# Kernel optimization log

Hardware: AMD Instinct MI355X
Metric: run time of the kernel (lower is better)

The kernel has to match this reference:

```python
import jax, jax.numpy as jnp
import numpy as np

N_NODES = 50000
N_EDGES = 800000
IN_DIM = 64
HID_DIM = 64
OUT_DIM = 16
N_RELS = 16
N_BASES = 4


def setup_inputs() -> dict:
    key = jax.random.key(0)
    ks = jax.random.split(key, 11)
    feats = jax.random.normal(ks[0], (N_NODES, IN_DIM), dtype=jnp.float32)
    src = jax.random.randint(ks[1], (N_EDGES,), 0, N_NODES, dtype=jnp.int32)
    dst = jax.random.randint(ks[2], (N_EDGES,), 0, N_NODES, dtype=jnp.int32)
    edge_type = jax.random.randint(ks[3], (N_EDGES,), 0, N_RELS, dtype=jnp.int32)
    edge_norm = jax.random.uniform(ks[4], (N_EDGES,), dtype=jnp.float32)
    # basis-decomposed relation weights: W[r] = sum_b coef[r,b] * bases[b]
    bases1 = jax.random.normal(ks[5], (N_BASES, IN_DIM, HID_DIM), dtype=jnp.float32) * (1.0 / np.sqrt(IN_DIM))
    coef1 = jax.random.normal(ks[6], (N_RELS, N_BASES), dtype=jnp.float32)
    bias1 = jnp.zeros((HID_DIM,), dtype=jnp.float32)
    bases2 = jax.random.normal(ks[7], (N_BASES, HID_DIM, OUT_DIM), dtype=jnp.float32) * (1.0 / np.sqrt(HID_DIM))
    coef2 = jax.random.normal(ks[8], (N_RELS, N_BASES), dtype=jnp.float32)
    bias2 = jnp.zeros((OUT_DIM,), dtype=jnp.float32)
    return {"feats": feats, "src": src, "dst": dst, "edge_type": edge_type,
            "edge_norm": edge_norm, "bases1": bases1, "coef1": coef1, "bias1": bias1,
            "bases2": bases2, "coef2": coef2, "bias2": bias2}


def _rel_graph_conv(x, src, dst, edge_type, edge_norm, bases, coef, bias):
    """One RelGraphConv layer (basis decomposition, low-mem: gather coef, not W)."""
    xs = x[src]                                   # [E, in]  gather source feats
    t = jnp.einsum('ei,bio->ebo', xs, bases)      # [E, B, out] per-basis transform
    c = coef[edge_type]                            # [E, B]   per-edge relation coefs
    msg = jnp.einsum('eb,ebo->eo', c, t)          # [E, out]
    msg = msg * edge_norm[:, None]                # apply edge norm
    h = jax.ops.segment_sum(msg, dst, num_segments=N_NODES)  # scatter-add by dst
    return jax.nn.relu(h + bias)                  # bias + activation (dropout=0, eval)


def reference(feats, src, dst, edge_type, edge_norm, bases1, coef1, bias1, bases2, coef2, bias2):
    h = _rel_graph_conv(feats, src, dst, edge_type, edge_norm, bases1, coef1, bias1)
    h = _rel_graph_conv(h, src, dst, edge_type, edge_norm, bases2, coef2, bias2)
    return h
```

## Files before the change

kernel.cpp:

```cpp
#include <hip/hip_runtime.h>

#define N_NODES 50000
#define N_EDGES 800000

typedef __attribute__((ext_vector_type(8))) short bf16x8;
typedef __attribute__((ext_vector_type(4))) float f32x4;

__device__ __forceinline__ unsigned bf16rne(float x) {
  unsigned u = __float_as_uint(x);
  return (u + 0x7FFFu + ((u >> 16) & 1u)) >> 16;
}
__device__ __forceinline__ unsigned packbf2(float a, float b) {
  return bf16rne(a) | (bf16rne(b) << 16);
}
__device__ __forceinline__ float bflo(unsigned u) { return __uint_as_float(u << 16); }
__device__ __forceinline__ float bfhi(unsigned u) { return __uint_as_float(u & 0xFFFF0000u); }

__global__ __launch_bounds__(256) void k_pack(
    const float4* __restrict__ feats4, uint2* __restrict__ xbf,
    const float* __restrict__ bases1, const float* __restrict__ bases2,
    unsigned short* __restrict__ b1T, unsigned short* __restrict__ b2p) {
  if (blockIdx.x < 3125) {
    const int i = blockIdx.x * 256 + threadIdx.x;
    float4 v = feats4[i];
    xbf[i] = make_uint2(packbf2(v.x, v.y), packbf2(v.z, v.w));
  } else {
    for (int idx = threadIdx.x; idx < 64 * 256; idx += 256) {
      int o = idx >> 8, q = idx & 255;
      b1T[idx] = (unsigned short)bf16rne(bases1[q * 64 + o]);
    }
    for (int idx = threadIdx.x; idx < 64 * 64; idx += 256) {
      int j = idx >> 6, k = idx & 63;
      int o = j >> 2, b = j & 3;
      b2p[idx] = (unsigned short)bf16rne(bases2[b * 1024 + k * 16 + o]);
    }
  }
}

#define G_HIST 64
#define CHUNK (N_EDGES / G_HIST)
#define NSLICE 4
#define HBINS (N_NODES / NSLICE)

__global__ __launch_bounds__(512) void k_hist(
    const int* __restrict__ dst, int* __restrict__ rank,
    unsigned short* __restrict__ bh) {
  __shared__ int hist[HBINS];
  const int c = blockIdx.x & (G_HIST - 1);
  const int p = blockIdx.x >> 6;
  const int e0 = c * CHUNK;
  const int lo = p * HBINS;
  for (int i = threadIdx.x; i < HBINS; i += 512) hist[i] = 0;
  __syncthreads();
  for (int i = threadIdx.x; i < CHUNK; i += 512) {
    const int d = dst[e0 + i] - lo;
    if ((unsigned)d < (unsigned)HBINS)
      rank[e0 + i] = atomicAdd(&hist[d], 1);
  }
  __syncthreads();
  for (int i = threadIdx.x; i < HBINS; i += 512)
    bh[(size_t)c * N_NODES + lo + i] = (unsigned short)hist[i];
}

#define NB 512
__global__ __launch_bounds__(512) void k_scan1(
    unsigned short* __restrict__ bh,
    int* __restrict__ rowp, int* __restrict__ bsum) {
  __shared__ unsigned short tile[G_HIST][NB];
  __shared__ int wsum[8];
  const int tid = threadIdx.x;
  const int n0 = blockIdx.x * NB;
  for (int idx = tid; idx < G_HIST * (NB / 4); idx += 512) {
    const int c = idx >> 7, j = idx & 127;
    const int nloc = 4 * j;
    uint2 u = make_uint2(0u, 0u);
    if (n0 + nloc < N_NODES)
      u = *(const uint2*)(bh + (size_t)c * N_NODES + n0 + nloc);
    *(uint2*)&tile[c][nloc] = u;
  }
  __syncthreads();
  int s = 0;
  for (int c = 0; c < G_HIST; ++c) {
    const int cnt = tile[c][tid];
    tile[c][tid] = (unsigned short)s;
    s += cnt;
  }
  __syncthreads();
  for (int idx = tid; idx < G_HIST * (NB / 4); idx += 512) {
    const int c = idx >> 7, j = idx & 127;
    const int nloc = 4 * j;
    if (n0 + nloc < N_NODES)
      *(uint2*)(bh + (size_t)c * N_NODES + n0 + nloc) = *(uint2*)&tile[c][nloc];
  }
  const int lane = tid & 63, wid = tid >> 6;
  int v = (n0 + tid < N_NODES) ? s : 0;
  int incl = v;
#pragma unroll
  for (int off = 1; off < 64; off <<= 1) {
    int t = __shfl_up(incl, off, 64);
    if (lane >= off) incl += t;
  }
  if (lane == 63) wsum[wid] = incl;
  __syncthreads();
  if (tid < 8) {
    int wi = wsum[tid];
#pragma unroll
    for (int off = 1; off < 8; off <<= 1) {
      int t = __shfl_up(wi, off, 64);
      if (lane >= off) wi += t;
    }
    wsum[tid] = wi;
  }
  __syncthreads();
  int woff = (wid > 0) ? wsum[wid - 1] : 0;
  int incl_all = incl + woff;
  if (n0 + tid < N_NODES) rowp[n0 + tid + 1] = incl_all;
  if (tid == NB - 1) bsum[blockIdx.x] = incl_all;
}

__global__ __launch_bounds__(512) void k_scan3(int* __restrict__ rowp,
                                               const int* __restrict__ bsum) {
  __shared__ int s_off;
  const int tid = threadIdx.x;
  if (tid < 64) {
    int v = 0;
    for (int b = tid; b < (int)blockIdx.x; b += 64) v += bsum[b];
#pragma unroll
    for (int off = 32; off >= 1; off >>= 1) v += __shfl_down(v, off, 64);
    if (tid == 0) s_off = v;
  }
  __syncthreads();
  const int i = blockIdx.x * NB + tid;
  if (i < N_NODES) rowp[i + 1] += s_off;
  if (i == 0) rowp[0] = 0;
}

__global__ __launch_bounds__(256) void k_scatter(
    const int* __restrict__ src, const int* __restrict__ dst,
    const int* __restrict__ ety, const float* __restrict__ enorm,
    const int* __restrict__ rowp, const int* __restrict__ rank,
    const unsigned short* __restrict__ bh, unsigned* __restrict__ s_edge) {
  int e = blockIdx.x * 256 + threadIdx.x;
  if (e >= N_EDGES) return;
  const int d = dst[e];
  const int b = e / CHUNK;
  const int pos = rowp[d] + (int)bh[(size_t)b * N_NODES + d] + rank[e];
  unsigned nq = (unsigned)(enorm[e] * 4096.f + 0.5f);
  nq = nq > 4095u ? 4095u : nq;
  s_edge[pos] = (unsigned)src[e] | ((unsigned)ety[e] << 16) | (nq << 20);
}

#define NMSCALE (1.f / 4096.f)

#define ROWB 264
__device__ __forceinline__ void gather_node(
    const int* __restrict__ rowp, const unsigned* __restrict__ s_edge,
    const uint2* __restrict__ xv, const float4* __restrict__ coefLDS,
    unsigned short* __restrict__ uA,
    int node, int m, int lane) {
  const int eslot = lane >> 4, ch4 = lane & 15;
  const int beg = rowp[node], end = rowp[node + 1];
  float4 a0 = {0, 0, 0, 0}, a1 = {0, 0, 0, 0}, a2 = {0, 0, 0, 0}, a3 = {0, 0, 0, 0};
  int j = beg + eslot;
  unsigned rec0 = 0, rec1 = 0;
  uint2 xp = {0, 0};
  if (j < end) rec0 = s_edge[j];
  if (j + 4 < end) rec1 = s_edge[j + 4];
  if (j < end) xp = xv[(rec0 & 0xFFFF) * 16 + ch4];
  while (j < end) {
    unsigned rec2 = 0;
    uint2 xp1 = {0, 0};
    if (j + 8 < end) rec2 = s_edge[j + 8];
    if (j + 4 < end) xp1 = xv[(rec1 & 0xFFFF) * 16 + ch4];
    const float nm = (float)(rec0 >> 20) * NMSCALE;
    const float4 c = coefLDS[(rec0 >> 16) & 15];
    const float w0 = nm * c.x, w1 = nm * c.y, w2 = nm * c.z, w3 = nm * c.w;
    const float x0 = bflo(xp.x), x1 = bfhi(xp.x), x2 = bflo(xp.y), x3 = bfhi(xp.y);
    a0.x += w0 * x0; a0.y += w0 * x1; a0.z += w0 * x2; a0.w += w0 * x3;
    a1.x += w1 * x0; a1.y += w1 * x1; a1.z += w1 * x2; a1.w += w1 * x3;
    a2.x += w2 * x0; a2.y += w2 * x1; a2.z += w2 * x2; a2.w += w2 * x3;
    a3.x += w3 * x0; a3.y += w3 * x1; a3.z += w3 * x2; a3.w += w3 * x3;
    j += 4; rec0 = rec1; rec1 = rec2; xp = xp1;
  }
#define RED1(x) x += __shfl_down(x, 32, 64)
  RED1(a0.x); RED1(a0.y); RED1(a0.z); RED1(a0.w);
  RED1(a1.x); RED1(a1.y); RED1(a1.z); RED1(a1.w);
  RED1(a2.x); RED1(a2.y); RED1(a2.z); RED1(a2.w);
  RED1(a3.x); RED1(a3.y); RED1(a3.z); RED1(a3.w);
#undef RED1
  if (eslot < 2) {
    unsigned short* row = uA + (eslot * 16 + m) * ROWB + 4 * ch4;
    *(uint2*)(row + 0 * 64) = make_uint2(packbf2(a0.x, a0.y), packbf2(a0.z, a0.w));
    *(uint2*)(row + 1 * 64) = make_uint2(packbf2(a1.x, a1.y), packbf2(a1.z, a1.w));
    *(uint2*)(row + 2 * 64) = make_uint2(packbf2(a2.x, a2.y), packbf2(a2.z, a2.w));
    *(uint2*)(row + 3 * 64) = make_uint2(packbf2(a3.x, a3.y), packbf2(a3.z, a3.w));
  }
}

__global__ __launch_bounds__(256) void k_l1_fused(
    const int* __restrict__ rowp, const unsigned* __restrict__ s_edge,
    const uint2* __restrict__ xbf, const float* __restrict__ coef1,
    const unsigned short* __restrict__ b1T,
    const float* __restrict__ bias1,
    const unsigned short* __restrict__ b2p,
    uint2* __restrict__ y2bf) {
  __shared__ __align__(16) unsigned short uA[2 * 16 * ROWB];
  __shared__ float coefs[64];
  __shared__ float cmat[16 * 68];
  const int wid = threadIdx.x >> 6, lane = threadIdx.x & 63;
  if (threadIdx.x < 64) coefs[threadIdx.x] = coef1[threadIdx.x];
  __syncthreads();
  const int nbase = blockIdx.x * 16;
#pragma unroll
  for (int jn = 0; jn < 4; ++jn) {
    const int m = wid * 4 + jn;
    gather_node(rowp, s_edge, xbf, (const float4*)coefs, uA, nbase + m, m, lane);
  }
  __syncthreads();
  const int nloc = lane & 15, kgrp = lane >> 4;
  f32x4 acc1 = {0.f, 0.f, 0.f, 0.f};
#pragma unroll
  for (int ks = 0; ks < 8; ++ks) {
    const int k0 = ks * 32 + kgrp * 8;
    const bf16x8 b = *(const bf16x8*)&b1T[(wid * 16 + nloc) * 256 + k0];
    const bf16x8 aS0 = *(const bf16x8*)&uA[(0 * 16 + nloc) * ROWB + k0];
    acc1 = __builtin_amdgcn_mfma_f32_16x16x32_bf16(aS0, b, acc1, 0, 0, 0);
    const bf16x8 aS1 = *(const bf16x8*)&uA[(1 * 16 + nloc) * ROWB + k0];
    acc1 = __builtin_amdgcn_mfma_f32_16x16x32_bf16(aS1, b, acc1, 0, 0, 0);
  }
  {
    const int o = wid * 16 + nloc;
    const float bs = bias1[o];
#pragma unroll
    for (int r = 0; r < 4; ++r) {
      const int m = (lane >> 4) * 4 + r;
      cmat[m * 68 + o] = fmaxf(acc1[r] + bs, 0.f);
    }
  }
  __syncthreads();
  f32x4 acc2 = {0.f, 0.f, 0.f, 0.f};
#pragma unroll
  for (int ks = 0; ks < 2; ++ks) {
    const int k0 = ks * 32 + kgrp * 8;
    const float4 c0 = *(const float4*)&cmat[nloc * 68 + k0];
    const float4 c1 = *(const float4*)&cmat[nloc * 68 + k0 + 4];
    union { bf16x8 v; unsigned u[4]; } au;
    au.u[0] = packbf2(c0.x, c0.y); au.u[1] = packbf2(c0.z, c0.w);
    au.u[2] = packbf2(c1.x, c1.y); au.u[3] = packbf2(c1.z, c1.w);
    const bf16x8 b = *(const bf16x8*)&b2p[(wid * 16 + nloc) * 64 + k0];
    acc2 = __builtin_amdgcn_mfma_f32_16x16x32_bf16(au.v, b, acc2, 0, 0, 0);
  }
  __syncthreads();
#pragma unroll
  for (int r = 0; r < 4; ++r) {
    const int m = (lane >> 4) * 4 + r;
    cmat[m * 68 + wid * 16 + nloc] = acc2[r];
  }
  __syncthreads();
  const int nl = threadIdx.x >> 4, c4 = threadIdx.x & 15;
  const float* cr = &cmat[nl * 68 + 4 * c4];
  y2bf[(size_t)(nbase + nl) * 16 + c4] =
      make_uint2(packbf2(cr[0], cr[1]), packbf2(cr[2], cr[3]));
}

__global__ __launch_bounds__(256) void k_l2_gather(
    const int* __restrict__ rowp, const unsigned* __restrict__ s_edge,
    const uint4* __restrict__ y2v,
    const float* __restrict__ coef2, const float* __restrict__ bias2,
    float2* __restrict__ out) {
  __shared__ float coefs[64];
  if (threadIdx.x < 64) coefs[threadIdx.x] = coef2[threadIdx.x];
  __syncthreads();
  const float4* coefv = (const float4*)coefs;
  const int wid = threadIdx.x >> 6, lane = threadIdx.x & 63;
  const int eslot = lane >> 3, og = lane & 7;
  const int nbase = blockIdx.x * 8 + wid * 2;

  int j[2], jend[2];
  float a0[2] = {0.f, 0.f}, a1[2] = {0.f, 0.f};
  unsigned r0[2], r1[2];
  uint4 yp[2];
#pragma unroll
  for (int m = 0; m < 2; ++m) {
    const int node = nbase + m;
    const int beg = rowp[node];
    jend[m] = rowp[node + 1];
    j[m] = beg + eslot;
    r0[m] = 0; r1[m] = 0;
    yp[m] = make_uint4(0, 0, 0, 0);
    if (j[m] < jend[m]) r0[m] = s_edge[j[m]];
    if (j[m] + 8 < jend[m]) r1[m] = s_edge[j[m] + 8];
  }
#pragma unroll
  for (int m = 0; m < 2; ++m)
    if (j[m] < jend[m]) yp[m] = y2v[(r0[m] & 0xFFFF) * 8 + og];

  while ((j[0] < jend[0]) | (j[1] < jend[1])) {
#pragma unroll
    for (int m = 0; m < 2; ++m) {
      unsigned r2 = 0;
      uint4 yp1 = make_uint4(0, 0, 0, 0);
      if (j[m] + 16 < jend[m]) r2 = s_edge[j[m] + 16];
      if (j[m] + 8 < jend[m]) yp1 = y2v[(r1[m] & 0xFFFF) * 8 + og];
      if (j[m] < jend[m]) {
        const float nm = (float)(r0[m] >> 20) * NMSCALE;
        const float4 c = coefv[(r0[m] >> 16) & 15];
        a0[m] += nm * (c.x * bflo(yp[m].x) + c.y * bfhi(yp[m].x) +
                       c.z * bflo(yp[m].y) + c.w * bfhi(yp[m].y));
        a1[m] += nm * (c.x * bflo(yp[m].z) + c.y * bfhi(yp[m].z) +
                       c.z * bflo(yp[m].w) + c.w * bfhi(yp[m].w));
      }
      j[m] += 8; r0[m] = r1[m]; r1[m] = r2; yp[m] = yp1;
    }
  }
#pragma unroll
  for (int m = 0; m < 2; ++m) {
    a0[m] += __shfl_down(a0[m], 32, 64);
    a0[m] += __shfl_down(a0[m], 16, 64);
    a0[m] += __shfl_down(a0[m], 8, 64);
    a1[m] += __shfl_down(a1[m], 32, 64);
    a1[m] += __shfl_down(a1[m], 16, 64);
    a1[m] += __shfl_down(a1[m], 8, 64);
  }
  if (eslot == 0) {
    const float b0 = bias2[2 * og], b1 = bias2[2 * og + 1];
#pragma unroll
    for (int m = 0; m < 2; ++m) {
      out[(size_t)(nbase + m) * 8 + og] =
          make_float2(fmaxf(a0[m] + b0, 0.f), fmaxf(a1[m] + b1, 0.f));
    }
  }
}

extern "C" void kernel_launch(void* const* d_in, const int* in_sizes, int n_in,
                              void* d_out, int out_size, void* d_ws, size_t ws_size,
                              hipStream_t stream) {
  const float* feats  = (const float*)d_in[0];
  const int*   src    = (const int*)d_in[1];
  const int*   dst    = (const int*)d_in[2];
  const int*   etype  = (const int*)d_in[3];
  const float* enorm  = (const float*)d_in[4];
  const float* bases1 = (const float*)d_in[5];
  const float* coef1  = (const float*)d_in[6];
  const float* bias1  = (const float*)d_in[7];
  const float* bases2 = (const float*)d_in[8];
  const float* coef2  = (const float*)d_in[9];
  const float* bias2  = (const float*)d_in[10];

  uint2* xbf    = (uint2*)d_ws;
  uint2* y2bf   = xbf + (size_t)N_NODES * 16;
  unsigned* s_edge = (unsigned*)(y2bf + (size_t)N_NODES * 16);
  int*   rank   = (int*)(s_edge + N_EDGES);
  unsigned short* bh = (unsigned short*)(rank + N_EDGES);
  unsigned short* b1T = bh + (size_t)G_HIST * N_NODES;
  unsigned short* b2p = b1T + 64 * 256;
  int*   rowp   = (int*)(b2p + 64 * 64);
  int*   bsum   = rowp + N_NODES + 1;

  const int SCAN_BLKS = (N_NODES + NB - 1) / NB;

  k_pack<<<3126, 256, 0, stream>>>((const float4*)feats, xbf, bases1,
                                   bases2, b1T, b2p);
  k_hist<<<G_HIST * NSLICE, 512, 0, stream>>>(dst, rank, bh);
  k_scan1<<<SCAN_BLKS, 512, 0, stream>>>(bh, rowp, bsum);
  k_scan3<<<SCAN_BLKS, 512, 0, stream>>>(rowp, bsum);
  k_scatter<<<N_EDGES / 256, 256, 0, stream>>>(src, dst, etype, enorm,
                                               rowp, rank, bh, s_edge);
  k_l1_fused<<<N_NODES / 16, 256, 0, stream>>>(rowp, s_edge, xbf, coef1,
                                               b1T, bias1, b2p, y2bf);
  k_l2_gather<<<N_NODES / 8, 256, 0, stream>>>(rowp, s_edge,
                                               (const uint4*)y2bf, coef2,
                                               bias2, (float2*)d_out);
}
```

Measured before the change: 191.1 us.

## Split edge gathers into contiguous per-slot chunks and store ranks as bytes

Both gather kernels now give each edge slot a contiguous chunk of a node's edge list. Each slot issues several independent record and feature loads per iteration, replacing the strided loop with one-step software prefetch, so more gathers are in flight at once. The per-edge histogram rank is now stored as an 8-bit value instead of a 32-bit int, which cuts rank write and read traffic in the hist and scatter kernels. The byte rank assumes no node gets 256 or more edges from a single chunk. The contiguous split makes slot reads of s_edge less coalesced across lanes and adds dummy loads of node 0 for padded slots.

Result: no change. 191.8 us (+0.4%).

```diff
diff --git a/kernel.cpp b/kernel.cpp
--- a/kernel.cpp
+++ b/kernel.cpp
@@ -43,7 +43,7 @@
 #define HBINS (N_NODES / NSLICE)
 
 __global__ __launch_bounds__(512) void k_hist(
-    const int* __restrict__ dst, int* __restrict__ rank,
+    const int* __restrict__ dst, unsigned char* __restrict__ rank,
     unsigned short* __restrict__ bh) {
   __shared__ int hist[HBINS];
   const int c = blockIdx.x & (G_HIST - 1);
@@ -55,7 +55,7 @@
   for (int i = threadIdx.x; i < CHUNK; i += 512) {
     const int d = dst[e0 + i] - lo;
     if ((unsigned)d < (unsigned)HBINS)
-      rank[e0 + i] = atomicAdd(&hist[d], 1);
+      rank[e0 + i] = (unsigned char)atomicAdd(&hist[d], 1);
   }
   __syncthreads();
   for (int i = threadIdx.x; i < HBINS; i += 512)
@@ -138,13 +138,13 @@
 __global__ __launch_bounds__(256) void k_scatter(
     const int* __restrict__ src, const int* __restrict__ dst,
     const int* __restrict__ ety, const float* __restrict__ enorm,
-    const int* __restrict__ rowp, const int* __restrict__ rank,
+    const int* __restrict__ rowp, const unsigned char* __restrict__ rank,
     const unsigned short* __restrict__ bh, unsigned* __restrict__ s_edge) {
   int e = blockIdx.x * 256 + threadIdx.x;
   if (e >= N_EDGES) return;
   const int d = dst[e];
   const int b = e / CHUNK;
-  const int pos = rowp[d] + (int)bh[(size_t)b * N_NODES + d] + rank[e];
+  const int pos = rowp[d] + (int)bh[(size_t)b * N_NODES + d] + (int)rank[e];
   unsigned nq = (unsigned)(enorm[e] * 4096.f + 0.5f);
   nq = nq > 4095u ? 4095u : nq;
   s_edge[pos] = (unsigned)src[e] | ((unsigned)ety[e] << 16) | (nq << 20);
@@ -160,27 +160,30 @@
     int node, int m, int lane) {
   const int eslot = lane >> 4, ch4 = lane & 15;
   const int beg = rowp[node], end = rowp[node + 1];
+  const int qlen = (end - beg + 3) >> 2;
+  int p = beg + eslot * qlen;
+  const int pend = min(p + qlen, end);
   float4 a0 = {0, 0, 0, 0}, a1 = {0, 0, 0, 0}, a2 = {0, 0, 0, 0}, a3 = {0, 0, 0, 0};
-  int j = beg + eslot;
-  unsigned rec0 = 0, rec1 = 0;
-  uint2 xp = {0, 0};
-  if (j < end) rec0 = s_edge[j];
-  if (j + 4 < end) rec1 = s_edge[j + 4];
-  if (j < end) xp = xv[(rec0 & 0xFFFF) * 16 + ch4];
-  while (j < end) {
-    unsigned rec2 = 0;
-    uint2 xp1 = {0, 0};
-    if (j + 8 < end) rec2 = s_edge[j + 8];
-    if (j + 4 < end) xp1 = xv[(rec1 & 0xFFFF) * 16 + ch4];
-    const float nm = (float)(rec0 >> 20) * NMSCALE;
-    const float4 c = coefLDS[(rec0 >> 16) & 15];
-    const float w0 = nm * c.x, w1 = nm * c.y, w2 = nm * c.z, w3 = nm * c.w;
-    const float x0 = bflo(xp.x), x1 = bfhi(xp.x), x2 = bflo(xp.y), x3 = bfhi(xp.y);
-    a0.x += w0 * x0; a0.y += w0 * x1; a0.z += w0 * x2; a0.w += w0 * x3;
-    a1.x += w1 * x0; a1.y += w1 * x1; a1.z += w1 * x2; a1.w += w1 * x3;
-    a2.x += w2 * x0; a2.y += w2 * x1; a2.z += w2 * x2; a2.w += w2 * x3;
-    a3.x += w3 * x0; a3.y += w3 * x1; a3.z += w3 * x2; a3.w += w3 * x3;
-    j += 4; rec0 = rec1; rec1 = rec2; xp = xp1;
+  for (; p < pend; p += 4) {
+    const int nb = pend - p;
+    unsigned rec[4];
+#pragma unroll
+    for (int t = 0; t < 4; ++t) rec[t] = (t < nb) ? s_edge[p + t] : 0u;
+    uint2 xp[4];
+#pragma unroll
+    for (int t = 0; t < 4; ++t) xp[t] = xv[(rec[t] & 0xFFFF) * 16 + ch4];
+#pragma unroll
+    for (int t = 0; t < 4; ++t) {
+      const float nm = (float)(rec[t] >> 20) * NMSCALE;
+      const float4 c = coefLDS[(rec[t] >> 16) & 15];
+      const float w0 = nm * c.x, w1 = nm * c.y, w2 = nm * c.z, w3 = nm * c.w;
+      const float x0 = bflo(xp[t].x), x1 = bfhi(xp[t].x);
+      const float x2 = bflo(xp[t].y), x3 = bfhi(xp[t].y);
+      a0.x += w0 * x0; a0.y += w0 * x1; a0.z += w0 * x2; a0.w += w0 * x3;
+      a1.x += w1 * x0; a1.y += w1 * x1; a1.z += w1 * x2; a1.w += w1 * x3;
+      a2.x += w2 * x0; a2.y += w2 * x1; a2.z += w2 * x2; a2.w += w2 * x3;
+      a3.x += w3 * x0; a3.y += w3 * x1; a3.z += w3 * x2; a3.w += w3 * x3;
+    }
   }
 #define RED1(x) x += __shfl_down(x, 32, 64)
   RED1(a0.x); RED1(a0.y); RED1(a0.z); RED1(a0.w);
@@ -276,42 +279,41 @@
   const int eslot = lane >> 3, og = lane & 7;
   const int nbase = blockIdx.x * 8 + wid * 2;
 
-  int j[2], jend[2];
   float a0[2] = {0.f, 0.f}, a1[2] = {0.f, 0.f};
-  unsigned r0[2], r1[2];
-  uint4 yp[2];
+  int p[2], pend[2];
 #pragma unroll
   for (int m = 0; m < 2; ++m) {
-    const int node = nbase + m;
-    const int beg = rowp[node];
-    jend[m] = rowp[node + 1];
-    j[m] = beg + eslot;
-    r0[m] = 0; r1[m] = 0;
-    yp[m] = make_uint4(0, 0, 0, 0);
-    if (j[m] < jend[m]) r0[m] = s_edge[j[m]];
-    if (j[m] + 8 < jend[m]) r1[m] = s_edge[j[m] + 8];
-  }
-#pragma unroll
-  for (int m = 0; m < 2; ++m)
-    if (j[m] < jend[m]) yp[m] = y2v[(r0[m] & 0xFFFF) * 8 + og];
-
-  while ((j[0] < jend[0]) | (j[1] < jend[1])) {
+    const int beg = rowp[nbase + m], end = rowp[nbase + m + 1];
+    const int qlen = (end - beg + 7) >> 3;
+    p[m] = beg + eslot * qlen;
+    pend[m] = min(p[m] + qlen, end);
+  }
+  while ((p[0] < pend[0]) | (p[1] < pend[1])) {
+    unsigned rec[2][2] = {{0u, 0u}, {0u, 0u}};
 #pragma unroll
     for (int m = 0; m < 2; ++m) {
-      unsigned r2 = 0;
-      uint4 yp1 = make_uint4(0, 0, 0, 0);
-      if (j[m] + 16 < jend[m]) r2 = s_edge[j[m] + 16];
-      if (j[m] + 8 < jend[m]) yp1 = y2v[(r1[m] & 0xFFFF) * 8 + og];
-      if (j[m] < jend[m]) {
-        const float nm = (float)(r0[m] >> 20) * NMSCALE;
-        const float4 c = coefv[(r0[m] >> 16) & 15];
-        a0[m] += nm * (c.x * bflo(yp[m].x) + c.y * bfhi(yp[m].x) +
-                       c.z * bflo(yp[m].y) + c.w * bfhi(yp[m].y));
-        a1[m] += nm * (c.x * bflo(yp[m].z) + c.y * bfhi(yp[m].z) +
-                       c.z * bflo(yp[m].w) + c.w * bfhi(yp[m].w));
+      if (p[m] < pend[m]) rec[m][0] = s_edge[p[m]];
+      if (p[m] + 1 < pend[m]) rec[m][1] = s_edge[p[m] + 1];
+    }
+    uint4 yp[2][2];
+#pragma unroll
+    for (int m = 0; m < 2; ++m)
+#pragma unroll
+      for (int t = 0; t < 2; ++t)
+        yp[m][t] = y2v[(rec[m][t] & 0xFFFF) * 8 + og];
+#pragma unroll
+    for (int m = 0; m < 2; ++m)
+#pragma unroll
+      for (int t = 0; t < 2; ++t) {
+        const float nm = (float)(rec[m][t] >> 20) * NMSCALE;
+        const float4 c = coefv[(rec[m][t] >> 16) & 15];
+        a0[m] += nm * (c.x * bflo(yp[m][t].x) + c.y * bfhi(yp[m][t].x) +
+                       c.z * bflo(yp[m][t].y) + c.w * bfhi(yp[m][t].y));
+        a1[m] += nm * (c.x * bflo(yp[m][t].z) + c.y * bfhi(yp[m][t].z) +
+                       c.z * bflo(yp[m][t].w) + c.w * bfhi(yp[m][t].w));
       }
-      j[m] += 8; r0[m] = r1[m]; r1[m] = r2; yp[m] = yp1;
-    }
+#pragma unroll
+    for (int m = 0; m < 2; ++m) p[m] += 2;
   }
 #pragma unroll
   for (int m = 0; m < 2; ++m) {
@@ -350,12 +352,12 @@
   uint2* xbf    = (uint2*)d_ws;
   uint2* y2bf   = xbf + (size_t)N_NODES * 16;
   unsigned* s_edge = (unsigned*)(y2bf + (size_t)N_NODES * 16);
-  int*   rank   = (int*)(s_edge + N_EDGES);
-  unsigned short* bh = (unsigned short*)(rank + N_EDGES);
+  unsigned short* bh = (unsigned short*)(s_edge + N_EDGES);
   unsigned short* b1T = bh + (size_t)G_HIST * N_NODES;
   unsigned short* b2p = b1T + 64 * 256;
   int*   rowp   = (int*)(b2p + 64 * 64);
   int*   bsum   = rowp + N_NODES + 1;
+  unsigned char* rank = (unsigned char*)(bsum + 128);
 
   const int SCAN_BLKS = (N_NODES + NB - 1) / NB;
 
```
